# Kernel tuning notes

Measured on AMD Instinct MI355X. Metric: run time of the kernel, lower is better.

The kernel has to match this reference:

```python
import jax, jax.numpy as jnp
import numpy as np

B, T, D = 4, 2048, 2048
H, DK, DV = 16, 128, 128


def setup_inputs() -> dict:
    key = jax.random.key(0)
    ks = jax.random.split(key, 8)
    s = 1.0 / np.sqrt(D)
    return {
        "q": jax.random.normal(ks[0], (B, T, D), jnp.float32),
        "k": jax.random.normal(ks[1], (B, T, D), jnp.float32),
        "v": jax.random.normal(ks[2], (B, T, D), jnp.float32),
        "mask": jnp.tril(jnp.ones((T, T), dtype=bool)),  # True = attend
        # weights stored as [in, out] (torch Linear applies x @ W.T)
        "Wq": jax.random.normal(ks[3], (D, H * DK), jnp.float32) * s,
        "Wk": jax.random.normal(ks[4], (D, H * DK), jnp.float32) * s,
        "Wv": jax.random.normal(ks[5], (D, H * DV), jnp.float32) * s,
        "Wo": jax.random.normal(ks[6], (H * DV, D), jnp.float32) * s,
    }


def _attention(q, k, v, mask, Wq, Wk, Wv, Wo):
    # project and split heads: [B,T,H*dh] -> [B,H,T,dh]
    def split_heads(x, dh):
        b, t, _ = x.shape
        return x.reshape(b, t, H, dh).transpose(0, 2, 1, 3)

    q_i = split_heads(q @ Wq, DK)
    k_i = split_heads(k @ Wk, DK)
    v_i = split_heads(v @ Wv, DV)

    scores = jnp.einsum("bhik,bhjk->bhij", q_i, k_i) / jnp.sqrt(
        jnp.asarray(DK, q_i.dtype)
    )
    neg = -jnp.finfo(scores.dtype).max
    scores = jnp.where(mask[None, None, :, :], scores, neg)
    attn = jax.nn.softmax(scores, axis=-1)
    vals = jnp.einsum("bhij,bhjv->bhiv", attn, v_i)  # [B,H,T,dv]
    merged = vals.transpose(0, 2, 1, 3).reshape(q.shape[0], q.shape[1], H * DV)
    return merged @ Wo


def reference(q, k, v, mask, Wq, Wk, Wv, Wo):
    return _attention(q, k, v, mask, Wq, Wk, Wv, Wo)
```

## Files before the change

kernel.cpp:

```cpp
#include <hip/hip_runtime.h>
#include <hip/hip_bf16.h>

typedef __attribute__((ext_vector_type(8))) short bf16x8;
typedef __attribute__((ext_vector_type(4))) unsigned short u16x4;
typedef __attribute__((ext_vector_type(4))) float f32x4;

constexpr int Bb = 4, Tt = 2048, Dd = 2048, Hh = 16, DHd = 128;

static __device__ __forceinline__ unsigned short f2bf(float f) {
  union { float f; unsigned u; } x; x.f = f;
  unsigned r = x.u + 0x7fffu + ((x.u >> 16) & 1u);
  return (unsigned short)(r >> 16);
}

static __device__ __forceinline__ void gld16(const void* g, void* l) {
  __builtin_amdgcn_global_load_lds(
      (__attribute__((address_space(1))) void*)g,
      (__attribute__((address_space(3))) void*)l, 16, 0, 0);
}

__global__ __launch_bounds__(256) void cvt_bf16(const float* __restrict__ s,
                                                unsigned short* __restrict__ d) {
  const size_t i = ((size_t)blockIdx.x * 256 + threadIdx.x) * 8;
  float4 a = *(const float4*)(s + i);
  float4 b = *(const float4*)(s + i + 4);
  bf16x8 pk;
  pk[0] = (short)f2bf(a.x); pk[1] = (short)f2bf(a.y);
  pk[2] = (short)f2bf(a.z); pk[3] = (short)f2bf(a.w);
  pk[4] = (short)f2bf(b.x); pk[5] = (short)f2bf(b.y);
  pk[6] = (short)f2bf(b.z); pk[7] = (short)f2bf(b.w);
  *(bf16x8*)(d + i) = pk;
}

__global__ __launch_bounds__(256) void wtrans_all(
    const float* __restrict__ Wq, const float* __restrict__ Wk,
    const float* __restrict__ Wv, const float* __restrict__ Wo,
    unsigned short* __restrict__ WqT, unsigned short* __restrict__ WkT,
    unsigned short* __restrict__ WvT, unsigned short* __restrict__ WoT,
    float qscale) {
  __shared__ __align__(16) unsigned short tile[64][72];
  const float* src;
  unsigned short* dst;
  float sc = 1.0f;
  switch (blockIdx.z) {
    case 0: src = Wq; dst = WqT; sc = qscale; break;
    case 1: src = Wk; dst = WkT; break;
    case 2: src = Wv; dst = WvT; break;
    default: src = Wo; dst = WoT; break;
  }
  const int t = threadIdx.x;
  const int k0 = blockIdx.x * 64, n0 = blockIdx.y * 64;
  const int c = t & 15, r = t >> 4;
#pragma unroll
  for (int p = 0; p < 4; ++p) {
    const int rr = r + 16 * p;
    float4 v = *(const float4*)(src + (size_t)(k0 + rr) * Dd + n0 + c * 4);
    u16x4 pk;
    pk[0] = f2bf(v.x * sc); pk[1] = f2bf(v.y * sc);
    pk[2] = f2bf(v.z * sc); pk[3] = f2bf(v.w * sc);
    *(u16x4*)&tile[rr][c * 4] = pk;
  }
  __syncthreads();
#pragma unroll
  for (int p = 0; p < 4; ++p) {
    const int nn = r + 16 * p;
    u16x4 pk;
    pk[0] = tile[c * 4 + 0][nn]; pk[1] = tile[c * 4 + 1][nn];
    pk[2] = tile[c * 4 + 2][nn]; pk[3] = tile[c * 4 + 3][nn];
    *(u16x4*)(dst + (size_t)(n0 + nn) * Dd + k0 + c * 4) = pk;
  }
}

template <int OMODE>
__global__ __launch_bounds__(512, 2) void gemm8p(
    const unsigned short* __restrict__ A, const unsigned short* __restrict__ Bt,
    void* __restrict__ Outp) {
  __shared__ __align__(16) unsigned short As[2][2][128 * 64];
  __shared__ __align__(16) unsigned short Bs[2][2][128 * 64];
  const int t = threadIdx.x, lane = t & 63, w = t >> 6;
  const int wm = w >> 2, wn = w & 3;
  const int fr = lane & 15, fq = lane >> 4;
  const int sw = fr & 7;
  const int slot = blockIdx.x;
  const int orig = (slot & 7) * 32 + (slot >> 3);
  const int m0 = (orig >> 3) * 256, n0 = (orig & 7) * 256;

  const int srow = t >> 3, sch = t & 7;
  const int scol = (sch ^ (srow & 7)) * 8;

  auto SA = [&](int tau, int h) {
    const unsigned short* g =
        A + (size_t)(m0 + h * 128 + srow) * Dd + tau * 64 + scol;
    unsigned short* l = &As[tau & 1][h][(srow * 8 + sch) * 8];
    gld16(g, l);
    gld16(g + (size_t)64 * Dd, l + 4096);
  };
  auto SB = [&](int tau, int h) {
    const unsigned short* g =
        Bt + (size_t)(n0 + h * 128 + srow) * Dd + tau * 64 + scol;
    unsigned short* l = &Bs[tau & 1][h][(srow * 8 + sch) * 8];
    gld16(g, l);
    gld16(g + (size_t)64 * Dd, l + 4096);
  };

  f32x4 acc[8][4] = {};
  constexpr int NT = Dd / 64;

  SB(0, 0); SB(0, 1); SA(0, 0); SA(0, 1);
  SB(1, 0); SB(1, 1); SA(1, 0); SA(1, 1);
  asm volatile("s_waitcnt vmcnt(8)" ::: "memory");
  __builtin_amdgcn_s_barrier();
  __builtin_amdgcn_sched_barrier(0);

  for (int tau = 0; tau < NT; ++tau) {
    const unsigned short* Ab = &As[tau & 1][wm][0];
    const unsigned short* Bb = &Bs[tau & 1][wn >> 1][0];
    const int brow = (wn & 1) * 64;

    bf16x8 a0[4][2], a1[4][2], b0[2][2], b1[2][2];

#pragma unroll
    for (int i = 0; i < 4; ++i)
#pragma unroll
      for (int ks = 0; ks < 2; ++ks)
        a0[i][ks] = *(const bf16x8*)&Ab[(i * 16 + fr) * 64 +
                                        (((ks * 4 + fq) ^ sw)) * 8];
#pragma unroll
    for (int j = 0; j < 2; ++j)
#pragma unroll
      for (int ks = 0; ks < 2; ++ks)
        b0[j][ks] = *(const bf16x8*)&Bb[(brow + j * 16 + fr) * 64 +
                                        (((ks * 4 + fq) ^ sw)) * 8];
    __builtin_amdgcn_s_barrier();
    __builtin_amdgcn_sched_barrier(0);
    __builtin_amdgcn_s_setprio(1);
#pragma unroll
    for (int i = 0; i < 4; ++i)
#pragma unroll
      for (int j = 0; j < 2; ++j)
#pragma unroll
        for (int ks = 0; ks < 2; ++ks)
          acc[i][j] = __builtin_amdgcn_mfma_f32_16x16x32_bf16(
              a0[i][ks], b0[j][ks], acc[i][j], 0, 0, 0);
    __builtin_amdgcn_s_setprio(0);
    __builtin_amdgcn_sched_barrier(0);
    __builtin_amdgcn_s_barrier();

#pragma unroll
    for (int j = 0; j < 2; ++j)
#pragma unroll
      for (int ks = 0; ks < 2; ++ks)
        b1[j][ks] = *(const bf16x8*)&Bb[(brow + (j + 2) * 16 + fr) * 64 +
                                        (((ks * 4 + fq) ^ sw)) * 8];
    __builtin_amdgcn_s_barrier();
    __builtin_amdgcn_sched_barrier(0);
    __builtin_amdgcn_s_setprio(1);
#pragma unroll
    for (int i = 0; i < 4; ++i)
#pragma unroll
      for (int j = 0; j < 2; ++j)
#pragma unroll
        for (int ks = 0; ks < 2; ++ks)
          acc[i][j + 2] = __builtin_amdgcn_mfma_f32_16x16x32_bf16(
              a0[i][ks], b1[j][ks], acc[i][j + 2], 0, 0, 0);
    __builtin_amdgcn_s_setprio(0);
    __builtin_amdgcn_sched_barrier(0);
    __builtin_amdgcn_s_barrier();

#pragma unroll
    for (int i = 0; i < 4; ++i)
#pragma unroll
      for (int ks = 0; ks < 2; ++ks)
        a1[i][ks] = *(const bf16x8*)&Ab[((i + 4) * 16 + fr) * 64 +
                                        (((ks * 4 + fq) ^ sw)) * 8];
    if (tau + 2 < NT) {
      SB(tau + 2, 0);
      SB(tau + 2, 1);
    }
    __builtin_amdgcn_s_barrier();
    __builtin_amdgcn_sched_barrier(0);
    __builtin_amdgcn_s_setprio(1);
#pragma unroll
    for (int i = 0; i < 4; ++i)
#pragma unroll
      for (int j = 0; j < 2; ++j)
#pragma unroll
        for (int ks = 0; ks < 2; ++ks)
          acc[i + 4][j] = __builtin_amdgcn_mfma_f32_16x16x32_bf16(
              a1[i][ks], b0[j][ks], acc[i + 4][j], 0, 0, 0);
    __builtin_amdgcn_s_setprio(0);
    __builtin_amdgcn_sched_barrier(0);
    __builtin_amdgcn_s_barrier();

    if (tau + 2 < NT) {
      SA(tau + 2, 0);
      SA(tau + 2, 1);
      asm volatile("s_waitcnt vmcnt(8)" ::: "memory");
    } else {
      asm volatile("s_waitcnt vmcnt(0)" ::: "memory");
    }
    __builtin_amdgcn_s_barrier();
    __builtin_amdgcn_sched_barrier(0);
    __builtin_amdgcn_s_setprio(1);
#pragma unroll
    for (int i = 0; i < 4; ++i)
#pragma unroll
      for (int j = 0; j < 2; ++j)
#pragma unroll
        for (int ks = 0; ks < 2; ++ks)
          acc[i + 4][j + 2] = __builtin_amdgcn_mfma_f32_16x16x32_bf16(
              a1[i][ks], b1[j][ks], acc[i + 4][j + 2], 0, 0, 0);
    __builtin_amdgcn_s_setprio(0);
    __builtin_amdgcn_sched_barrier(0);
    __builtin_amdgcn_s_barrier();
  }

#pragma unroll
  for (int m = 0; m < 8; ++m) {
    const int mg = m0 + wm * 128 + m * 16 + fq * 4;
    const int bb = mg >> 11, tt0 = mg & (Tt - 1);
#pragma unroll
    for (int n = 0; n < 4; ++n) {
      const int ng = n0 + wn * 64 + n * 16 + fr;
      if (OMODE == 0) {
        float* o = (float*)Outp + (size_t)mg * Dd + ng;
#pragma unroll
        for (int r = 0; r < 4; ++r) o[(size_t)r * Dd] = acc[m][n][r];
      } else if (OMODE == 1) {
        const int h = ng >> 7, dh = ng & 127;
        unsigned short* o = (unsigned short*)Outp +
                            (((size_t)bb * Hh + h) * Tt + tt0) * DHd + dh;
#pragma unroll
        for (int r = 0; r < 4; ++r) o[r * DHd] = f2bf(acc[m][n][r]);
      } else {
        const int h = ng >> 7, dh = ng & 127;
        u16x4 pk;
#pragma unroll
        for (int r = 0; r < 4; ++r) pk[r] = f2bf(acc[m][n][r]);
        *(u16x4*)((unsigned short*)Outp +
                  (((size_t)bb * Hh + h) * DHd + dh) * Tt + tt0) = pk;
      }
    }
  }
}

__global__ __launch_bounds__(512, 2) void fattn(
    const unsigned short* __restrict__ Qp, const unsigned short* __restrict__ Kp,
    const unsigned short* __restrict__ Vt, unsigned short* __restrict__ Ao) {
  __shared__ __align__(16) unsigned short Ks[2][64 * 128];
  __shared__ __align__(16) unsigned short Vs[2][128 * 64];
  const int t = threadIdx.x, lane = t & 63, w = t >> 6;
  const int fr = lane & 15, fq = lane >> 4;
  const int rsw = fr & 7;
  const int id = blockIdx.x;
  const int xcd = id & 7, slot = id >> 3;
  const int s5 = slot >> 5, r_ = slot & 31;
  const int bh = xcd * 8 + (r_ >> 2);
  const int q2 = r_ & 3;
  const int qb = s5 ? q2 : 7 - q2;
  const int q0w = qb * 256 + w * 32;
  const unsigned short* Qb = Qp + (size_t)bh * Tt * DHd;
  const unsigned short* Kb = Kp + (size_t)bh * Tt * DHd;
  const unsigned short* Vb = Vt + (size_t)bh * DHd * Tt;

  bf16x8 qf[2][4];
#pragma unroll
  for (int mg = 0; mg < 2; ++mg)
#pragma unroll
    for (int ks = 0; ks < 4; ++ks)
      qf[mg][ks] = *(const bf16x8*)(Qb + (size_t)(q0w + mg * 16 + fr) * DHd +
                                    ks * 32 + fq * 8);

  f32x4 oacc[2][8] = {};
  float m_[2] = {-1e30f, -1e30f};
  float l_[2] = {0.f, 0.f};

  auto STAGE = [&](int b, int kv0) {
#pragma unroll
    for (int p = 0; p < 2; ++p) {
      const int idx = t + p * 512, row = idx >> 4, ch = idx & 15;
      gld16(Kb + (size_t)(kv0 + row) * DHd + ((ch ^ (row & 7)) * 8),
            &Ks[b][idx * 8]);
    }
#pragma unroll
    for (int p = 0; p < 2; ++p) {
      const int idx = t + p * 512, row = idx >> 3, ch = idx & 7;
      gld16(Vb + (size_t)row * Tt + kv0 + ((ch ^ (row & 7)) * 8),
            &Vs[b][idx * 8]);
    }
  };

  const int ntile = 4 * qb + 4;
  STAGE(0, 0);
  int cur = 0;

  for (int kt = 0; kt < ntile; ++kt) {
    const int kv0 = kt * 64;
    __builtin_amdgcn_s_barrier();
    if (kt + 1 < ntile) {
      STAGE(cur ^ 1, (kt + 1) * 64);
      asm volatile("s_waitcnt vmcnt(4)" ::: "memory");
    } else {
      asm volatile("s_waitcnt vmcnt(0)" ::: "memory");
    }
    __builtin_amdgcn_sched_barrier(0);
    __builtin_amdgcn_s_barrier();

    if (kv0 <= q0w + 31) {
      const unsigned short* Kc = &Ks[cur][0];
      const unsigned short* Vc = &Vs[cur][0];

      f32x4 s[2][4] = {};
      __builtin_amdgcn_s_setprio(1);
#pragma unroll
      for (int tt = 0; tt < 4; ++tt) {
        bf16x8 kf[4];
#pragma unroll
        for (int ks = 0; ks < 4; ++ks)
          kf[ks] = *(const bf16x8*)(Kc + (tt * 16 + fr) * 128 +
                                    ((ks * 4 + fq) ^ rsw) * 8);
#pragma unroll
        for (int ks = 0; ks < 4; ++ks) {
          s[0][tt] = __builtin_amdgcn_mfma_f32_16x16x32_bf16(kf[ks], qf[0][ks],
                                                             s[0][tt], 0, 0, 0);
          s[1][tt] = __builtin_amdgcn_mfma_f32_16x16x32_bf16(kf[ks], qf[1][ks],
                                                             s[1][tt], 0, 0, 0);
        }
      }
      __builtin_amdgcn_s_setprio(0);

      uint2 c[2][4];
#pragma unroll
      for (int mg = 0; mg < 2; ++mg) {
        const int qg = q0w + mg * 16;
        if (kv0 + 63 > qg) {
          const int qa = qg + fr;
#pragma unroll
          for (int tt = 0; tt < 4; ++tt)
#pragma unroll
            for (int r = 0; r < 4; ++r)
              if (kv0 + tt * 16 + fq * 4 + r > qa) s[mg][tt][r] = -1e30f;
        }

        float tmax = s[mg][0][0];
#pragma unroll
        for (int tt = 0; tt < 4; ++tt)
#pragma unroll
          for (int r = 0; r < 4; ++r) tmax = fmaxf(tmax, s[mg][tt][r]);
        tmax = fmaxf(tmax, __shfl_xor(tmax, 16));
        tmax = fmaxf(tmax, __shfl_xor(tmax, 32));

        if (!__all(tmax <= m_[mg] + 8.0f)) {
          const float mn = fmaxf(m_[mg], tmax);
          const float alpha = __builtin_amdgcn_exp2f(m_[mg] - mn);
          m_[mg] = mn;
          float al4[4];
#pragma unroll
          for (int r = 0; r < 4; ++r) al4[r] = __shfl(alpha, fq * 4 + r);
#pragma unroll
          for (int dt = 0; dt < 8; ++dt)
#pragma unroll
            for (int r = 0; r < 4; ++r) oacc[mg][dt][r] *= al4[r];
          l_[mg] *= alpha;
        }

        float rs = 0.f;
#pragma unroll
        for (int tt = 0; tt < 4; ++tt)
#pragma unroll
          for (int r = 0; r < 4; ++r) {
            const float p = __builtin_amdgcn_exp2f(s[mg][tt][r] - m_[mg]);
            s[mg][tt][r] = p;
            rs += p;
          }
        rs += __shfl_xor(rs, 16);
        rs += __shfl_xor(rs, 32);
        l_[mg] += rs;

#pragma unroll
        for (int tt = 0; tt < 4; ++tt) {
          unsigned r0, r1;
          asm("v_cvt_pk_bf16_f32 %0, %1, %2"
              : "=v"(r0) : "v"(s[mg][tt][0]), "v"(s[mg][tt][1]));
          asm("v_cvt_pk_bf16_f32 %0, %1, %2"
              : "=v"(r1) : "v"(s[mg][tt][2]), "v"(s[mg][tt][3]));
          c[mg][tt].x = r0; c[mg][tt].y = r1;
        }
      }

      const int src0 = fr + 32 * (fq & 1);
      const int src1 = src0 + 16;
      const bool hi = (fq >> 1) != 0;
      __builtin_amdgcn_s_setprio(1);
#pragma unroll
      for (int ks2 = 0; ks2 < 2; ++ks2) {
        bf16x8 pf[2];
#pragma unroll
        for (int mg = 0; mg < 2; ++mg) {
          const int a0 = __shfl((int)c[mg][2 * ks2].x, src0);
          const int b0 = __shfl((int)c[mg][2 * ks2 + 1].x, src0);
          const int a1 = __shfl((int)c[mg][2 * ks2].y, src0);
          const int b1 = __shfl((int)c[mg][2 * ks2 + 1].y, src0);
          const int a2 = __shfl((int)c[mg][2 * ks2].x, src1);
          const int b2 = __shfl((int)c[mg][2 * ks2 + 1].x, src1);
          const int a3 = __shfl((int)c[mg][2 * ks2].y, src1);
          const int b3 = __shfl((int)c[mg][2 * ks2 + 1].y, src1);
          union { int wd[4]; bf16x8 v; } pu;
          pu.wd[0] = hi ? b0 : a0;
          pu.wd[1] = hi ? b1 : a1;
          pu.wd[2] = hi ? b2 : a2;
          pu.wd[3] = hi ? b3 : a3;
          pf[mg] = pu.v;
        }
#pragma unroll
        for (int dt = 0; dt < 8; ++dt) {
          const bf16x8 vf = *(const bf16x8*)(Vc + (dt * 16 + fr) * 64 +
                                             ((ks2 * 4 + fq) ^ rsw) * 8);
          oacc[0][dt] = __builtin_amdgcn_mfma_f32_16x16x32_bf16(pf[0], vf,
                                                                oacc[0][dt], 0, 0, 0);
          oacc[1][dt] = __builtin_amdgcn_mfma_f32_16x16x32_bf16(pf[1], vf,
                                                                oacc[1][dt], 0, 0, 0);
        }
      }
      __builtin_amdgcn_s_setprio(0);
    }
    cur ^= 1;
  }

  const int bb = bh >> 4, hh = bh & 15;
#pragma unroll
  for (int mg = 0; mg < 2; ++mg) {
    float linv[4];
#pragma unroll
    for (int r = 0; r < 4; ++r) linv[r] = 1.0f / __shfl(l_[mg], fq * 4 + r);
    const int qrow = q0w + mg * 16 + fq * 4;
#pragma unroll
    for (int r = 0; r < 4; ++r) {
      unsigned short* o = Ao + ((size_t)bb * Tt + qrow + r) * Dd + hh * DHd + fr;
#pragma unroll
      for (int dt = 0; dt < 8; ++dt) o[dt * 16] = f2bf(oacc[mg][dt][r] * linv[r]);
    }
  }
}

extern "C" void kernel_launch(void* const* d_in, const int* in_sizes, int n_in,
                              void* d_out, int out_size, void* d_ws, size_t ws_size,
                              hipStream_t stream) {
  const float* q = (const float*)d_in[0];
  const float* k = (const float*)d_in[1];
  const float* v = (const float*)d_in[2];
  const float* Wq = (const float*)d_in[4];
  const float* Wk = (const float*)d_in[5];
  const float* Wv = (const float*)d_in[6];
  const float* Wo = (const float*)d_in[7];

  const size_t WE = (size_t)Dd * Dd;
  const size_t PE = (size_t)Bb * Hh * Tt * DHd;
  unsigned short* WqT = (unsigned short*)d_ws;
  unsigned short* WkT = WqT + WE;
  unsigned short* WvT = WkT + WE;
  unsigned short* WoT = WvT + WE;
  unsigned short* Qx = WoT + WE;
  unsigned short* Kx = Qx + PE;
  unsigned short* Vx = Kx + PE;
  unsigned short* Ax = Vx + PE;

  const float qscale = (float)(1.4426950408889634 / 11.313708498984761);
  wtrans_all<<<dim3(32, 32, 4), 256, 0, stream>>>(
      Wq, Wk, Wv, Wo, WqT, WkT, WvT, WoT, qscale);

  cvt_bf16<<<dim3(8192), 256, 0, stream>>>(q, Ax);
  gemm8p<1><<<dim3(256), 512, 0, stream>>>(Ax, WqT, Qx);
  cvt_bf16<<<dim3(8192), 256, 0, stream>>>(k, Ax);
  gemm8p<1><<<dim3(256), 512, 0, stream>>>(Ax, WkT, Kx);
  cvt_bf16<<<dim3(8192), 256, 0, stream>>>(v, Ax);
  gemm8p<2><<<dim3(256), 512, 0, stream>>>(Ax, WvT, Vx);
  fattn<<<dim3(512), 512, 0, stream>>>(Qx, Kx, Vx, Ax);
  gemm8p<0><<<dim3(256), 512, 0, stream>>>(Ax, WoT, (float*)d_out);
}
```

Before: 478.2 us.

## Fuse fp32-to-bf16 activation conversion into projection GEMM A-tile loading

Removes the three standalone cvt_bf16 passes over q, k and v. A new GEMM variant reads fp32 activations straight into registers, converts them to bf16 and writes swizzled tiles to LDS, pipelined one stage ahead. B still streams through global_load_lds. This saves a write and re-read of a bf16 copy of each input and three kernel launches. In exchange it doubles the global A-traffic per tile and adds register pressure and VALU conversion work inside the GEMM main loop.

```diff
diff --git a/kernel.cpp b/kernel.cpp
--- a/kernel.cpp
+++ b/kernel.cpp
@@ -17,19 +17,6 @@
   __builtin_amdgcn_global_load_lds(
       (__attribute__((address_space(1))) void*)g,
       (__attribute__((address_space(3))) void*)l, 16, 0, 0);
-}
-
-__global__ __launch_bounds__(256) void cvt_bf16(const float* __restrict__ s,
-                                                unsigned short* __restrict__ d) {
-  const size_t i = ((size_t)blockIdx.x * 256 + threadIdx.x) * 8;
-  float4 a = *(const float4*)(s + i);
-  float4 b = *(const float4*)(s + i + 4);
-  bf16x8 pk;
-  pk[0] = (short)f2bf(a.x); pk[1] = (short)f2bf(a.y);
-  pk[2] = (short)f2bf(a.z); pk[3] = (short)f2bf(a.w);
-  pk[4] = (short)f2bf(b.x); pk[5] = (short)f2bf(b.y);
-  pk[6] = (short)f2bf(b.z); pk[7] = (short)f2bf(b.w);
-  *(bf16x8*)(d + i) = pk;
 }
 
 __global__ __launch_bounds__(256) void wtrans_all(
@@ -72,9 +59,206 @@
 }
 
 template <int OMODE>
+__global__ __launch_bounds__(512, 2) void gemm8pF(
+    const float* __restrict__ Afp, const unsigned short* __restrict__ Bt,
+    void* __restrict__ Outp) {
+  __shared__ __align__(16) unsigned short As[2][2][128 * 64];
+  __shared__ __align__(16) unsigned short Bs[2][2][128 * 64];
+  const int t = threadIdx.x, lane = t & 63, w = t >> 6;
+  const int wm = w >> 2, wn = w & 3;
+  const int fr = lane & 15, fq = lane >> 4;
+  const int sw = fr & 7;
+  const int slot = blockIdx.x;
+  const int orig = (slot & 7) * 32 + (slot >> 3);
+  const int m0 = (orig >> 3) * 256, n0 = (orig & 7) * 256;
+
+  const int srow = t >> 3, sch = t & 7;
+  const int scol = (sch ^ (srow & 7)) * 8;
+  auto SB = [&](int tau, int h) {
+    const unsigned short* g =
+        Bt + (size_t)(n0 + h * 128 + srow) * Dd + tau * 64 + scol;
+    unsigned short* l = &Bs[tau & 1][h][(srow * 8 + sch) * 8];
+    gld16(g, l);
+    gld16(g + (size_t)64 * Dd, l + 4096);
+  };
+
+  const int arow = (t >> 1) & 127;
+  const int ah = t >> 8;
+  const int ag0 = (t & 1) * 4;
+  float4 areg[8];
+  auto ALOAD = [&](int tau) {
+    const float* g = Afp + (size_t)(m0 + ah * 128 + arow) * Dd + tau * 64 + ag0 * 8;
+#pragma unroll
+    for (int i = 0; i < 8; ++i) areg[i] = *(const float4*)(g + i * 4);
+  };
+  auto AWRITE = [&](int tau) {
+    unsigned short* base = &As[tau & 1][ah][arow * 64];
+#pragma unroll
+    for (int c2 = 0; c2 < 4; ++c2) {
+      bf16x8 pk;
+      pk[0] = (short)f2bf(areg[2 * c2].x); pk[1] = (short)f2bf(areg[2 * c2].y);
+      pk[2] = (short)f2bf(areg[2 * c2].z); pk[3] = (short)f2bf(areg[2 * c2].w);
+      pk[4] = (short)f2bf(areg[2 * c2 + 1].x); pk[5] = (short)f2bf(areg[2 * c2 + 1].y);
+      pk[6] = (short)f2bf(areg[2 * c2 + 1].z); pk[7] = (short)f2bf(areg[2 * c2 + 1].w);
+      *(bf16x8*)(base + (((ag0 + c2) ^ (arow & 7)) * 8)) = pk;
+    }
+  };
+
+  f32x4 acc[8][4] = {};
+  constexpr int NT = Dd / 64;
+
+  SB(0, 0); SB(0, 1);
+  __builtin_amdgcn_sched_barrier(0);
+  ALOAD(0);
+  __builtin_amdgcn_sched_barrier(0);
+  SB(1, 0); SB(1, 1);
+  __builtin_amdgcn_sched_barrier(0);
+  asm volatile("s_waitcnt vmcnt(4)" ::: "memory");
+  AWRITE(0);
+  __builtin_amdgcn_sched_barrier(0);
+  ALOAD(1);
+  __builtin_amdgcn_sched_barrier(0);
+  asm volatile("s_waitcnt lgkmcnt(0)" ::: "memory");
+  __builtin_amdgcn_sched_barrier(0);
+  __builtin_amdgcn_s_barrier();
+  __builtin_amdgcn_sched_barrier(0);
+
+  for (int tau = 0; tau < NT; ++tau) {
+    const unsigned short* Ab = &As[tau & 1][wm][0];
+    const unsigned short* Bb = &Bs[tau & 1][wn >> 1][0];
+    const int brow = (wn & 1) * 64;
+
+    bf16x8 a0[4][2], a1[4][2], b0[2][2], b1[2][2];
+
+#pragma unroll
+    for (int i = 0; i < 4; ++i)
+#pragma unroll
+      for (int ks = 0; ks < 2; ++ks)
+        a0[i][ks] = *(const bf16x8*)&Ab[(i * 16 + fr) * 64 +
+                                        (((ks * 4 + fq) ^ sw)) * 8];
+#pragma unroll
+    for (int j = 0; j < 2; ++j)
+#pragma unroll
+      for (int ks = 0; ks < 2; ++ks)
+        b0[j][ks] = *(const bf16x8*)&Bb[(brow + j * 16 + fr) * 64 +
+                                        (((ks * 4 + fq) ^ sw)) * 8];
+    __builtin_amdgcn_s_barrier();
+    __builtin_amdgcn_sched_barrier(0);
+    __builtin_amdgcn_s_setprio(1);
+#pragma unroll
+    for (int i = 0; i < 4; ++i)
+#pragma unroll
+      for (int j = 0; j < 2; ++j)
+#pragma unroll
+        for (int ks = 0; ks < 2; ++ks)
+          acc[i][j] = __builtin_amdgcn_mfma_f32_16x16x32_bf16(
+              a0[i][ks], b0[j][ks], acc[i][j], 0, 0, 0);
+    __builtin_amdgcn_s_setprio(0);
+    __builtin_amdgcn_sched_barrier(0);
+    __builtin_amdgcn_s_barrier();
+
+#pragma unroll
+    for (int j = 0; j < 2; ++j)
+#pragma unroll
+      for (int ks = 0; ks < 2; ++ks)
+        b1[j][ks] = *(const bf16x8*)&Bb[(brow + (j + 2) * 16 + fr) * 64 +
+                                        (((ks * 4 + fq) ^ sw)) * 8];
+    __builtin_amdgcn_s_barrier();
+    __builtin_amdgcn_sched_barrier(0);
+    __builtin_amdgcn_s_setprio(1);
+#pragma unroll
+    for (int i = 0; i < 4; ++i)
+#pragma unroll
+      for (int j = 0; j < 2; ++j)
+#pragma unroll
+        for (int ks = 0; ks < 2; ++ks)
+          acc[i][j + 2] = __builtin_amdgcn_mfma_f32_16x16x32_bf16(
+              a0[i][ks], b1[j][ks], acc[i][j + 2], 0, 0, 0);
+    __builtin_amdgcn_s_setprio(0);
+    __builtin_amdgcn_sched_barrier(0);
+    __builtin_amdgcn_s_barrier();
+
+#pragma unroll
+    for (int i = 0; i < 4; ++i)
+#pragma unroll
+      for (int ks = 0; ks < 2; ++ks)
+        a1[i][ks] = *(const bf16x8*)&Ab[((i + 4) * 16 + fr) * 64 +
+                                        (((ks * 4 + fq) ^ sw)) * 8];
+    if (tau + 2 < NT) SB(tau + 2, 0);
+    __builtin_amdgcn_s_barrier();
+    __builtin_amdgcn_sched_barrier(0);
+    __builtin_amdgcn_s_setprio(1);
+#pragma unroll
+    for (int i = 0; i < 4; ++i)
+#pragma unroll
+      for (int j = 0; j < 2; ++j)
+#pragma unroll
+        for (int ks = 0; ks < 2; ++ks)
+          acc[i + 4][j] = __builtin_amdgcn_mfma_f32_16x16x32_bf16(
+              a1[i][ks], b0[j][ks], acc[i + 4][j], 0, 0, 0);
+    __builtin_amdgcn_s_setprio(0);
+    __builtin_amdgcn_sched_barrier(0);
+    __builtin_amdgcn_s_barrier();
+
+    if (tau + 2 < NT) {
+      SB(tau + 2, 1);
+      __builtin_amdgcn_sched_barrier(0);
+      asm volatile("s_waitcnt vmcnt(4)" ::: "memory");
+      AWRITE(tau + 1);
+      __builtin_amdgcn_sched_barrier(0);
+      ALOAD(tau + 2);
+      __builtin_amdgcn_sched_barrier(0);
+      asm volatile("s_waitcnt lgkmcnt(0)" ::: "memory");
+    } else if (tau + 1 < NT) {
+      asm volatile("s_waitcnt vmcnt(0)" ::: "memory");
+      AWRITE(tau + 1);
+      __builtin_amdgcn_sched_barrier(0);
+      asm volatile("s_waitcnt lgkmcnt(0)" ::: "memory");
+    }
+    __builtin_amdgcn_sched_barrier(0);
+    __builtin_amdgcn_s_barrier();
+    __builtin_amdgcn_sched_barrier(0);
+    __builtin_amdgcn_s_setprio(1);
+#pragma unroll
+    for (int i = 0; i < 4; ++i)
+#pragma unroll
+      for (int j = 0; j < 2; ++j)
+#pragma unroll
+        for (int ks = 0; ks < 2; ++ks)
+          acc[i + 4][j + 2] = __builtin_amdgcn_mfma_f32_16x16x32_bf16(
+              a1[i][ks], b1[j][ks], acc[i + 4][j + 2], 0, 0, 0);
+    __builtin_amdgcn_s_setprio(0);
+    __builtin_amdgcn_sched_barrier(0);
+    __builtin_amdgcn_s_barrier();
+  }
+
+#pragma unroll
+  for (int m = 0; m < 8; ++m) {
+    const int mg = m0 + wm * 128 + m * 16 + fq * 4;
+    const int bb = mg >> 11, tt0 = mg & (Tt - 1);
+#pragma unroll
+    for (int n = 0; n < 4; ++n) {
+      const int ng = n0 + wn * 64 + n * 16 + fr;
+      const int h = ng >> 7, dh = ng & 127;
+      if (OMODE == 1) {
+        unsigned short* o = (unsigned short*)Outp +
+                            (((size_t)bb * Hh + h) * Tt + tt0) * DHd + dh;
+#pragma unroll
+        for (int r = 0; r < 4; ++r) o[r * DHd] = f2bf(acc[m][n][r]);
+      } else {
+        u16x4 pk;
+#pragma unroll
+        for (int r = 0; r < 4; ++r) pk[r] = f2bf(acc[m][n][r]);
+        *(u16x4*)((unsigned short*)Outp +
+                  (((size_t)bb * Hh + h) * DHd + dh) * Tt + tt0) = pk;
+      }
+    }
+  }
+}
+
 __global__ __launch_bounds__(512, 2) void gemm8p(
     const unsigned short* __restrict__ A, const unsigned short* __restrict__ Bt,
-    void* __restrict__ Outp) {
+    float* __restrict__ Outp) {
   __shared__ __align__(16) unsigned short As[2][2][128 * 64];
   __shared__ __align__(16) unsigned short Bs[2][2][128 * 64];
   const int t = threadIdx.x, lane = t & 63, w = t >> 6;
@@ -218,28 +402,12 @@
 #pragma unroll
   for (int m = 0; m < 8; ++m) {
     const int mg = m0 + wm * 128 + m * 16 + fq * 4;
-    const int bb = mg >> 11, tt0 = mg & (Tt - 1);
 #pragma unroll
     for (int n = 0; n < 4; ++n) {
       const int ng = n0 + wn * 64 + n * 16 + fr;
-      if (OMODE == 0) {
-        float* o = (float*)Outp + (size_t)mg * Dd + ng;
-#pragma unroll
-        for (int r = 0; r < 4; ++r) o[(size_t)r * Dd] = acc[m][n][r];
-      } else if (OMODE == 1) {
-        const int h = ng >> 7, dh = ng & 127;
-        unsigned short* o = (unsigned short*)Outp +
-                            (((size_t)bb * Hh + h) * Tt + tt0) * DHd + dh;
-#pragma unroll
-        for (int r = 0; r < 4; ++r) o[r * DHd] = f2bf(acc[m][n][r]);
-      } else {
-        const int h = ng >> 7, dh = ng & 127;
-        u16x4 pk;
-#pragma unroll
-        for (int r = 0; r < 4; ++r) pk[r] = f2bf(acc[m][n][r]);
-        *(u16x4*)((unsigned short*)Outp +
-                  (((size_t)bb * Hh + h) * DHd + dh) * Tt + tt0) = pk;
-      }
+      float* o = Outp + (size_t)mg * Dd + ng;
+#pragma unroll
+      for (int r = 0; r < 4; ++r) o[(size_t)r * Dd] = acc[m][n][r];
     }
   }
 }
@@ -469,12 +637,9 @@
   wtrans_all<<<dim3(32, 32, 4), 256, 0, stream>>>(
       Wq, Wk, Wv, Wo, WqT, WkT, WvT, WoT, qscale);
 
-  cvt_bf16<<<dim3(8192), 256, 0, stream>>>(q, Ax);
-  gemm8p<1><<<dim3(256), 512, 0, stream>>>(Ax, WqT, Qx);
-  cvt_bf16<<<dim3(8192), 256, 0, stream>>>(k, Ax);
-  gemm8p<1><<<dim3(256), 512, 0, stream>>>(Ax, WkT, Kx);
-  cvt_bf16<<<dim3(8192), 256, 0, stream>>>(v, Ax);
-  gemm8p<2><<<dim3(256), 512, 0, stream>>>(Ax, WvT, Vx);
+  gemm8pF<1><<<dim3(256), 512, 0, stream>>>(q, WqT, Qx);
+  gemm8pF<1><<<dim3(256), 512, 0, stream>>>(k, WkT, Kx);
+  gemm8pF<2><<<dim3(256), 512, 0, stream>>>(v, WvT, Vx);
   fattn<<<dim3(512), 512, 0, stream>>>(Qx, Kx, Vx, Ax);
-  gemm8p<0><<<dim3(256), 512, 0, stream>>>(Ax, WoT, (float*)d_out);
+  gemm8p<<<dim3(256), 512, 0, stream>>>(Ax, WoT, (float*)d_out);
 }
```

Result: slower. 628.0 us (+31.3%).
